# Kernel tuning notes

Measured on AMD Instinct MI355X. Metric: run time of the kernel, lower is better.

## Reference

```python
import jax, jax.numpy as jnp
import numpy as np

EMBED_DIM = 1024
NUM_HEADS = 16
HEAD_DIM = EMBED_DIM // NUM_HEADS
ROPE_BASE = 10000.0


def setup_inputs() -> dict:
    key = jax.random.key(0)
    ks = jax.random.split(key, 5)
    B, S, D = 2, 2048, EMBED_DIM
    # kaiming_uniform_(a=sqrt(5)) on [out, in] -> bound = 1/sqrt(in)
    bound = 1.0 / np.sqrt(D)
    x = jax.random.normal(ks[0], (B, S, D), dtype=jnp.float32)
    Wq = jax.random.uniform(ks[1], (D, D), dtype=jnp.float32, minval=-bound, maxval=bound)
    Wk = jax.random.uniform(ks[2], (D, D), dtype=jnp.float32, minval=-bound, maxval=bound)
    Wv = jax.random.uniform(ks[3], (D, D), dtype=jnp.float32, minval=-bound, maxval=bound)
    Wo = jax.random.uniform(ks[4], (D, D), dtype=jnp.float32, minval=-bound, maxval=bound)
    return {"x": x, "Wq": Wq, "Wk": Wk, "Wv": Wv, "Wo": Wo}


def _rope(t):
    # t: [B, H, S, hd]; standard half-split RoPE, base 10000
    hd = t.shape[-1]
    half = hd // 2
    S = t.shape[2]
    inv_freq = 1.0 / (ROPE_BASE ** (jnp.arange(half, dtype=jnp.float32) / half))
    ang = jnp.arange(S, dtype=jnp.float32)[:, None] * inv_freq[None, :]  # [S, half]
    cos, sin = jnp.cos(ang), jnp.sin(ang)
    t1, t2 = t[..., :half], t[..., half:]
    return jnp.concatenate([t1 * cos - t2 * sin, t1 * sin + t2 * cos], axis=-1)


def _attention_mc(x, Wq, Wk, Wv, Wo):
    B, S, D = x.shape
    H, hd = NUM_HEADS, HEAD_DIM
    # Linear layers: y = x @ W.T (no bias)
    q = (x @ Wq.T).reshape(B, S, H, hd).transpose(0, 2, 1, 3)  # [B,H,S,hd]
    k = (x @ Wk.T).reshape(B, S, H, hd).transpose(0, 2, 1, 3)
    v = (x @ Wv.T).reshape(B, S, H, hd).transpose(0, 2, 1, 3)
    q = _rope(q)
    k = _rope(k)
    scale = 1.0 / jnp.sqrt(jnp.float32(hd))
    scores = jnp.einsum("bhqd,bhkd->bhqk", q, k) * scale  # [B,H,S,S]
    causal = jnp.tril(jnp.ones((S, S), dtype=bool))
    scores = jnp.where(causal, scores, jnp.finfo(scores.dtype).min)
    attn = jax.nn.softmax(scores, axis=-1)
    out = jnp.einsum("bhqk,bhkd->bhqd", attn, v)  # [B,H,S,hd]
    out = out.transpose(0, 2, 1, 3).reshape(B, S, D)
    return out @ Wo.T


def reference(x, Wq, Wk, Wv, Wo):
    return _attention_mc(x, Wq, Wk, Wv, Wo)
```

## Files before the change

kernel.cpp:

```cpp
#include <hip/hip_runtime.h>
#include <math.h>
#include <stdint.h>


#define S_LEN 2048
#define NHEAD 16
#define HDIM  64
#define NBH   32

typedef __attribute__((ext_vector_type(8))) short  bf16x8;
typedef __attribute__((ext_vector_type(4))) float  f32x4;
typedef unsigned short u16;
typedef unsigned int   u32;

__device__ __forceinline__ u16 f2bf(float f) {
    u32 u = __float_as_uint(f);
    return (u16)((u + 0x7FFFu + ((u >> 16) & 1u)) >> 16);
}
__device__ __forceinline__ float bf2f(u16 s) {
    return __uint_as_float(((u32)s) << 16);
}
__device__ __forceinline__ f32x4 mfma16(bf16x8 a, bf16x8 b, f32x4 c) {
    return __builtin_amdgcn_mfma_f32_16x16x32_bf16(a, b, c, 0, 0, 0);
}
__device__ __forceinline__ void gll16(const void* g, void* l) {
    __builtin_amdgcn_global_load_lds((const __attribute__((address_space(1))) u32*)g,
                                     (__attribute__((address_space(3))) u32*)l, 16, 0, 0);
}

__global__ __launch_bounds__(256)
void split_convert(const float* __restrict__ x,
                   const float* __restrict__ Wq, const float* __restrict__ Wk,
                   const float* __restrict__ Wv, const float* __restrict__ Wo,
                   u16* __restrict__ xhi, u16* __restrict__ xlo,
                   u16* __restrict__ whi, u16* __restrict__ wlo)
{
    const int g = blockIdx.x * 256 + threadIdx.x;
    const float* src; u16 *dhi, *dlo; int loc;
    if (g < 1048576) { src = x; dhi = xhi; dlo = xlo; loc = g; }
    else {
        const int r = g - 1048576;
        const int wsel = r >> 18;
        loc = r & 262143;
        src = (wsel == 0) ? Wq : (wsel == 1) ? Wk : (wsel == 2) ? Wv : Wo;
        dhi = whi + ((size_t)wsel << 20);
        dlo = wlo + ((size_t)wsel << 20);
    }
    const float4 v = reinterpret_cast<const float4*>(src)[loc];
    ushort4 hv, lv;
    hv.x = f2bf(v.x); lv.x = f2bf(v.x - bf2f(hv.x));
    hv.y = f2bf(v.y); lv.y = f2bf(v.y - bf2f(hv.y));
    hv.z = f2bf(v.z); lv.z = f2bf(v.z - bf2f(hv.z));
    hv.w = f2bf(v.w); lv.w = f2bf(v.w - bf2f(hv.w));
    reinterpret_cast<ushort4*>(dhi)[loc] = hv;
    reinterpret_cast<ushort4*>(dlo)[loc] = lv;
}

__global__ __launch_bounds__(256)
void qkv_mfma(const u16* __restrict__ xhi, const u16* __restrict__ xlo,
              const u16* __restrict__ whi, const u16* __restrict__ wlo,
              u16* __restrict__ qhi, u16* __restrict__ qlo,
              u16* __restrict__ khi, u16* __restrict__ klo,
              u16* __restrict__ vhi, u16* __restrict__ vlo)
{
    __shared__ __align__(16) u16 Ah[4096], Al[4096], Bh[4096], Bl[4096];
    const int tid = threadIdx.x, lane = tid & 63, w = tid >> 6;
    const int l15 = lane & 15, l16 = lane >> 4;
    const int m0 = blockIdx.x * 128;
    const int ng = blockIdx.y * 128;
    const int tsel = ng >> 10;
    const int nloc0 = ng & 1023;
    const u16* __restrict__ Wh = whi + ((size_t)tsel << 20);
    const u16* __restrict__ Wl = wlo + ((size_t)tsel << 20);

    f32x4 acc[4][4];
    #pragma unroll
    for (int i = 0; i < 4; ++i)
        #pragma unroll
        for (int j = 0; j < 4; ++j) acc[i][j] = (f32x4){0.f, 0.f, 0.f, 0.f};

    for (int k0 = 0; k0 < 1024; k0 += 32) {
        __syncthreads();
        #pragma unroll
        for (int c = 0; c < 2; ++c) {
            const int idx  = w * 2 + c;
            const int trow = idx * 16 + (lane >> 2);
            const int tcol = (lane & 3) * 8;
            const size_t ga = (size_t)(m0 + trow) * 1024 + k0 + tcol;
            const size_t gb = (size_t)(nloc0 + trow) * 1024 + k0 + tcol;
            gll16(xhi + ga, (char*)Ah + idx * 1024);
            gll16(xlo + ga, (char*)Al + idx * 1024);
            gll16(Wh + gb,  (char*)Bh + idx * 1024);
            gll16(Wl + gb,  (char*)Bl + idx * 1024);
        }
        __syncthreads();
        const int mo = (w >> 1) * 64, no = (w & 1) * 64;
        bf16x8 a_h[4], a_l[4], b_h[4], b_l[4];
        #pragma unroll
        for (int f = 0; f < 4; ++f) {
            const int ao = (mo + f * 16 + l15) * 32 + l16 * 8;
            a_h[f] = *(const bf16x8*)&Ah[ao];
            a_l[f] = *(const bf16x8*)&Al[ao];
            const int bo = (no + f * 16 + l15) * 32 + l16 * 8;
            b_h[f] = *(const bf16x8*)&Bh[bo];
            b_l[f] = *(const bf16x8*)&Bl[bo];
        }
        #pragma unroll
        for (int i = 0; i < 4; ++i)
            #pragma unroll
            for (int j = 0; j < 4; ++j) {
                acc[i][j] = mfma16(a_h[i], b_h[j], acc[i][j]);
                acc[i][j] = mfma16(a_h[i], b_l[j], acc[i][j]);
                acc[i][j] = mfma16(a_l[i], b_h[j], acc[i][j]);
            }
    }

    const int mo = (w >> 1) * 64, no = (w & 1) * 64;
    const int hh = (nloc0 + no) >> 6;
    if (tsel < 2) {
        u16* __restrict__ dh = tsel ? khi : qhi;
        u16* __restrict__ dl = tsel ? klo : qlo;
        const float scl = tsel ? 1.0f : 0.125f;
        #pragma unroll
        for (int i = 0; i < 4; ++i)
            #pragma unroll
            for (int e = 0; e < 4; ++e) {
                const int row = m0 + mo + i * 16 + l16 * 4 + e;
                const int s = row & 2047, b = row >> 11;
                const size_t base = ((size_t)(b * NHEAD + hh) * S_LEN + s) * HDIM;
                #pragma unroll
                for (int j = 0; j < 2; ++j) {
                    const int d = j * 16 + l15;
                    const float inv = (float)exp((double)d * -0.28782313662425574);
                    const float ang = (float)s * inv;
                    const float sn = sinf(ang), cs = cosf(ang);
                    const float x1 = acc[i][j][e], x2 = acc[i][j + 2][e];
                    const float o1 = (x1 * cs - x2 * sn) * scl;
                    const float o2 = (x1 * sn + x2 * cs) * scl;
                    const u16 h1 = f2bf(o1), h2 = f2bf(o2);
                    dh[base + d]      = h1;
                    dl[base + d]      = f2bf(o1 - bf2f(h1));
                    dh[base + d + 32] = h2;
                    dl[base + d + 32] = f2bf(o2 - bf2f(h2));
                }
            }
    } else {
        #pragma unroll
        for (int i = 0; i < 4; ++i)
            #pragma unroll
            for (int e = 0; e < 4; ++e) {
                const int row = m0 + mo + i * 16 + l16 * 4 + e;
                const int s = row & 2047, b = row >> 11;
                const size_t base = ((size_t)(b * NHEAD + hh) * S_LEN + s) * HDIM;
                #pragma unroll
                for (int j = 0; j < 4; ++j) {
                    const float o = acc[i][j][e];
                    const u16 h1 = f2bf(o);
                    vhi[base + j * 16 + l15] = h1;
                    vlo[base + j * 16 + l15] = f2bf(o - bf2f(h1));
                }
            }
    }
}

__global__ __launch_bounds__(256)
void vtrans(const u16* __restrict__ vhi, const u16* __restrict__ vlo,
            u16* __restrict__ vthi, u16* __restrict__ vtlo)
{
    __shared__ __align__(16) u16 T[64][72];
    const u16* __restrict__ src = blockIdx.z ? vlo : vhi;
    u16* __restrict__ dst = blockIdx.z ? vtlo : vthi;
    const int bh = blockIdx.y;
    const int s0 = blockIdx.x * 64;
    const int tid = threadIdx.x;
    #pragma unroll
    for (int p = 0; p < 2; ++p) {
        const int c = tid + p * 256;
        const int r = c >> 3, dc = (c & 7) * 8;
        *(uint4*)&T[r][dc] = *(const uint4*)&src[((size_t)bh * S_LEN + s0 + r) * HDIM + dc];
    }
    __syncthreads();
    #pragma unroll
    for (int p = 0; p < 2; ++p) {
        const int c = tid + p * 256;
        const int d = c >> 3, sc8 = (c & 7) * 8;
        __align__(16) u16 tmp[8];
        #pragma unroll
        for (int u = 0; u < 8; ++u) tmp[u] = T[sc8 + u][d];
        *(uint4*)&dst[((size_t)bh * HDIM + d) * S_LEN + s0 + sc8] = *(uint4*)tmp;
    }
}

__global__ __launch_bounds__(256)
void attn_mfma(const u16* __restrict__ qhi, const u16* __restrict__ qlo,
               const u16* __restrict__ khi, const u16* __restrict__ klo,
               const u16* __restrict__ vthi, const u16* __restrict__ vtlo,
               u16* __restrict__ ohi, u16* __restrict__ olo)
{
    __shared__ __align__(16) u16 Kh[64][72], Kl[64][72], Vh[64][72], Vl[64][72];
    __shared__ __align__(16) float Pw[4][16][68];
    const int tid = threadIdx.x, lane = tid & 63, w = tid >> 6;
    const int l15 = lane & 15, l16 = lane >> 4;
    const int qt = blockIdx.x, bh = blockIdx.y;
    const size_t sbase = (size_t)bh * S_LEN * HDIM;
    const size_t dbase = (size_t)bh * HDIM * S_LEN;

    bf16x8 q_h[2], q_l[2];
    {
        const int s = qt * 64 + w * 16 + l15;
        #pragma unroll
        for (int ks = 0; ks < 2; ++ks) {
            const size_t ga = sbase + (size_t)s * HDIM + ks * 32 + l16 * 8;
            q_h[ks] = *(const bf16x8*)&qhi[ga];
            q_l[ks] = *(const bf16x8*)&qlo[ga];
        }
    }

    f32x4 oacc[4];
    #pragma unroll
    for (int t = 0; t < 4; ++t) oacc[t] = (f32x4){0.f, 0.f, 0.f, 0.f};
    float m_i[4], l_i[4];
    #pragma unroll
    for (int e = 0; e < 4; ++e) { m_i[e] = -INFINITY; l_i[e] = 0.f; }

    for (int kt = 0; kt <= qt; ++kt) {
        __syncthreads();
        #pragma unroll
        for (int p = 0; p < 2; ++p) {
            const int c = tid + p * 256;
            const int r = c >> 3, dc = (c & 7) * 8;
            const size_t gk = sbase + (size_t)(kt * 64 + r) * HDIM + dc;
            *(uint4*)&Kh[r][dc] = *(const uint4*)&khi[gk];
            *(uint4*)&Kl[r][dc] = *(const uint4*)&klo[gk];
            const size_t gv = dbase + (size_t)r * S_LEN + kt * 64 + dc;
            *(uint4*)&Vh[r][dc] = *(const uint4*)&vthi[gv];
            *(uint4*)&Vl[r][dc] = *(const uint4*)&vtlo[gv];
        }
        __syncthreads();

        f32x4 st[4];
        #pragma unroll
        for (int t = 0; t < 4; ++t) st[t] = (f32x4){0.f, 0.f, 0.f, 0.f};
        #pragma unroll
        for (int t = 0; t < 4; ++t)
            #pragma unroll
            for (int ks = 0; ks < 2; ++ks) {
                const bf16x8 kf_h = *(const bf16x8*)&Kh[t * 16 + l15][ks * 32 + l16 * 8];
                const bf16x8 kf_l = *(const bf16x8*)&Kl[t * 16 + l15][ks * 32 + l16 * 8];
                st[t] = mfma16(q_h[ks], kf_h, st[t]);
                st[t] = mfma16(q_h[ks], kf_l, st[t]);
                st[t] = mfma16(q_l[ks], kf_h, st[t]);
            }
        if (kt == qt) {
            #pragma unroll
            for (int t = 0; t < 4; ++t)
                #pragma unroll
                for (int e = 0; e < 4; ++e)
                    if (t * 16 + l15 > w * 16 + l16 * 4 + e) st[t][e] = -1e30f;
        }
        #pragma unroll
        for (int e = 0; e < 4; ++e) {
            float mx = fmaxf(fmaxf(st[0][e], st[1][e]), fmaxf(st[2][e], st[3][e]));
            #pragma unroll
            for (int msk = 8; msk >= 1; msk >>= 1) mx = fmaxf(mx, __shfl_xor(mx, msk));
            const float mn = fmaxf(m_i[e], mx);
            const float scl = __expf(m_i[e] - mn);
            float rs = 0.f;
            #pragma unroll
            for (int t = 0; t < 4; ++t) {
                const float p = __expf(st[t][e] - mn);
                st[t][e] = p; rs += p;
            }
            #pragma unroll
            for (int msk = 8; msk >= 1; msk >>= 1) rs += __shfl_xor(rs, msk);
            l_i[e] = l_i[e] * scl + rs;
            m_i[e] = mn;
            #pragma unroll
            for (int t = 0; t < 4; ++t) oacc[t][e] *= scl;
        }
        #pragma unroll
        for (int t = 0; t < 4; ++t)
            #pragma unroll
            for (int e = 0; e < 4; ++e)
                Pw[w][l16 * 4 + e][t * 16 + l15] = st[t][e];
        bf16x8 p_h[2], p_l[2];
        #pragma unroll
        for (int ks = 0; ks < 2; ++ks) {
            float pf[8];
            *(f32x4*)&pf[0] = *(const f32x4*)&Pw[w][l15][ks * 32 + l16 * 8];
            *(f32x4*)&pf[4] = *(const f32x4*)&Pw[w][l15][ks * 32 + l16 * 8 + 4];
            #pragma unroll
            for (int u = 0; u < 8; ++u) {
                const u16 hb = f2bf(pf[u]);
                p_h[ks][u] = (short)hb;
                p_l[ks][u] = (short)f2bf(pf[u] - bf2f(hb));
            }
        }
        #pragma unroll
        for (int t = 0; t < 4; ++t)
            #pragma unroll
            for (int ks = 0; ks < 2; ++ks) {
                const bf16x8 vf_h = *(const bf16x8*)&Vh[t * 16 + l15][ks * 32 + l16 * 8];
                const bf16x8 vf_l = *(const bf16x8*)&Vl[t * 16 + l15][ks * 32 + l16 * 8];
                oacc[t] = mfma16(p_h[ks], vf_h, oacc[t]);
                oacc[t] = mfma16(p_h[ks], vf_l, oacc[t]);
                oacc[t] = mfma16(p_l[ks], vf_h, oacc[t]);
            }
    }
    #pragma unroll
    for (int e = 0; e < 4; ++e) {
        const float inv = 1.f / l_i[e];
        const int s = qt * 64 + w * 16 + l16 * 4 + e;
        #pragma unroll
        for (int t = 0; t < 4; ++t) {
            const float o = oacc[t][e] * inv;
            const size_t ga = sbase + (size_t)s * HDIM + t * 16 + l15;
            const u16 hb = f2bf(o);
            ohi[ga] = hb;
            olo[ga] = f2bf(o - bf2f(hb));
        }
    }
}

__global__ __launch_bounds__(256)
void proj_mfma(const u16* __restrict__ ahi, const u16* __restrict__ alo,
               const u16* __restrict__ wohi, const u16* __restrict__ wolo,
               float* __restrict__ out)
{
    __shared__ __align__(16) u16 Ah[4096], Al[4096], Bh[4096], Bl[4096];
    const int tid = threadIdx.x, lane = tid & 63, w = tid >> 6;
    const int l15 = lane & 15, l16 = lane >> 4;
    const int m0 = blockIdx.x * 128, n0 = blockIdx.y * 128;

    f32x4 acc[4][4];
    #pragma unroll
    for (int i = 0; i < 4; ++i)
        #pragma unroll
        for (int j = 0; j < 4; ++j) acc[i][j] = (f32x4){0.f, 0.f, 0.f, 0.f};

    for (int k0 = 0; k0 < 1024; k0 += 32) {
        __syncthreads();
        #pragma unroll
        for (int c = 0; c < 2; ++c) {
            const int idx  = w * 2 + c;
            const int trow = idx * 16 + (lane >> 2);
            const int tcol = (lane & 3) * 8;
            const int ri = m0 + trow;
            const int b = ri >> 11, s = ri & 2047;
            const int kc = k0 + tcol;
            const int hh = kc >> 6, dd = kc & 63;
            const size_t ga = ((size_t)(b * NHEAD + hh) * S_LEN + s) * HDIM + dd;
            const size_t gb = (size_t)(n0 + trow) * 1024 + k0 + tcol;
            gll16(ahi + ga,  (char*)Ah + idx * 1024);
            gll16(alo + ga,  (char*)Al + idx * 1024);
            gll16(wohi + gb, (char*)Bh + idx * 1024);
            gll16(wolo + gb, (char*)Bl + idx * 1024);
        }
        __syncthreads();
        const int mo = (w >> 1) * 64, no = (w & 1) * 64;
        bf16x8 a_h[4], a_l[4], b_h[4], b_l[4];
        #pragma unroll
        for (int f = 0; f < 4; ++f) {
            const int ao = (mo + f * 16 + l15) * 32 + l16 * 8;
            a_h[f] = *(const bf16x8*)&Ah[ao];
            a_l[f] = *(const bf16x8*)&Al[ao];
            const int bo = (no + f * 16 + l15) * 32 + l16 * 8;
            b_h[f] = *(const bf16x8*)&Bh[bo];
            b_l[f] = *(const bf16x8*)&Bl[bo];
        }
        #pragma unroll
        for (int i = 0; i < 4; ++i)
            #pragma unroll
            for (int j = 0; j < 4; ++j) {
                acc[i][j] = mfma16(a_h[i], b_h[j], acc[i][j]);
                acc[i][j] = mfma16(a_h[i], b_l[j], acc[i][j]);
                acc[i][j] = mfma16(a_l[i], b_h[j], acc[i][j]);
            }
    }
    const int mo = (w >> 1) * 64, no = (w & 1) * 64;
    #pragma unroll
    for (int i = 0; i < 4; ++i)
        #pragma unroll
        for (int e = 0; e < 4; ++e) {
            const int row = m0 + mo + i * 16 + l16 * 4 + e;
            #pragma unroll
            for (int j = 0; j < 4; ++j)
                out[(size_t)row * 1024 + n0 + no + j * 16 + l15] = acc[i][j][e];
        }
}

extern "C" void kernel_launch(void* const* d_in, const int* in_sizes, int n_in,
                              void* d_out, int out_size, void* d_ws, size_t ws_size,
                              hipStream_t stream)
{
    const float* x  = (const float*)d_in[0];
    const float* Wq = (const float*)d_in[1];
    const float* Wk = (const float*)d_in[2];
    const float* Wv = (const float*)d_in[3];
    const float* Wo = (const float*)d_in[4];
    float* out = (float*)d_out;

    char* ws = (char*)d_ws;
    const size_t MB = (size_t)1 << 20;
    u16* xhi  = (u16*)(ws +  0 * MB);
    u16* xlo  = (u16*)(ws +  8 * MB);
    u16* whi  = (u16*)(ws + 16 * MB);
    u16* wlo  = (u16*)(ws + 24 * MB);
    u16* qhi  = (u16*)(ws + 32 * MB);
    u16* qlo  = (u16*)(ws + 40 * MB);
    u16* khi  = (u16*)(ws + 48 * MB);
    u16* klo  = (u16*)(ws + 56 * MB);
    u16* vhi  = (u16*)(ws + 64 * MB);
    u16* vlo  = (u16*)(ws + 72 * MB);
    u16* vthi = (u16*)(ws + 80 * MB);
    u16* vtlo = (u16*)(ws + 88 * MB);

    split_convert<<<8192, 256, 0, stream>>>(x, Wq, Wk, Wv, Wo, xhi, xlo, whi, wlo);
    qkv_mfma<<<dim3(32, 24), 256, 0, stream>>>(xhi, xlo, whi, wlo,
                                               qhi, qlo, khi, klo, vhi, vlo);
    vtrans<<<dim3(32, NBH, 2), 256, 0, stream>>>(vhi, vlo, vthi, vtlo);
    attn_mfma<<<dim3(32, NBH), 256, 0, stream>>>(qhi, qlo, khi, klo, vthi, vtlo,
                                                 xhi, xlo);
    proj_mfma<<<dim3(32, 8), 256, 0, stream>>>(xhi, xlo,
                                               whi + ((size_t)3 << 20), wlo + ((size_t)3 << 20),
                                               out);
}
```

Before: 600.0 us.

## Fuse V transpose into QKV epilogue and stage stores through LDS

The QKV GEMM epilogue now writes through shared memory so global stores of Q/K and of attention output become 16-byte coalesced rows. V is written directly in transposed layout, which removes the separate vtrans kernel and its round trip through global memory. The attention grid is also reversed so the heaviest causal query tiles launch first, for better load balance. In exchange it adds an extra barrier and an LDS staging pass in each epilogue, and the shared-memory buffers are aliased.

```diff
diff --git a/kernel.cpp b/kernel.cpp
--- a/kernel.cpp
+++ b/kernel.cpp
@@ -61,9 +61,9 @@
               const u16* __restrict__ whi, const u16* __restrict__ wlo,
               u16* __restrict__ qhi, u16* __restrict__ qlo,
               u16* __restrict__ khi, u16* __restrict__ klo,
-              u16* __restrict__ vhi, u16* __restrict__ vlo)
+              u16* __restrict__ vthi, u16* __restrict__ vtlo)
 {
-    __shared__ __align__(16) u16 Ah[4096], Al[4096], Bh[4096], Bl[4096];
+    __shared__ __align__(16) u16 SMEM[20480];
     const int tid = threadIdx.x, lane = tid & 63, w = tid >> 6;
     const int l15 = lane & 15, l16 = lane >> 4;
     const int m0 = blockIdx.x * 128;
@@ -88,10 +88,10 @@
             const int tcol = (lane & 3) * 8;
             const size_t ga = (size_t)(m0 + trow) * 1024 + k0 + tcol;
             const size_t gb = (size_t)(nloc0 + trow) * 1024 + k0 + tcol;
-            gll16(xhi + ga, (char*)Ah + idx * 1024);
-            gll16(xlo + ga, (char*)Al + idx * 1024);
-            gll16(Wh + gb,  (char*)Bh + idx * 1024);
-            gll16(Wl + gb,  (char*)Bl + idx * 1024);
+            gll16(xhi + ga, (char*)SMEM + idx * 1024);
+            gll16(xlo + ga, (char*)SMEM +  8192 + idx * 1024);
+            gll16(Wh + gb,  (char*)SMEM + 16384 + idx * 1024);
+            gll16(Wl + gb,  (char*)SMEM + 24576 + idx * 1024);
         }
         __syncthreads();
         const int mo = (w >> 1) * 64, no = (w & 1) * 64;
@@ -99,11 +99,11 @@
         #pragma unroll
         for (int f = 0; f < 4; ++f) {
             const int ao = (mo + f * 16 + l15) * 32 + l16 * 8;
-            a_h[f] = *(const bf16x8*)&Ah[ao];
-            a_l[f] = *(const bf16x8*)&Al[ao];
+            a_h[f] = *(const bf16x8*)&SMEM[ao];
+            a_l[f] = *(const bf16x8*)&SMEM[4096 + ao];
             const int bo = (no + f * 16 + l15) * 32 + l16 * 8;
-            b_h[f] = *(const bf16x8*)&Bh[bo];
-            b_l[f] = *(const bf16x8*)&Bl[bo];
+            b_h[f] = *(const bf16x8*)&SMEM[8192 + bo];
+            b_l[f] = *(const bf16x8*)&SMEM[12288 + bo];
         }
         #pragma unroll
         for (int i = 0; i < 4; ++i)
@@ -115,79 +115,84 @@
             }
     }
 
+    __syncthreads();
     const int mo = (w >> 1) * 64, no = (w & 1) * 64;
     const int hh = (nloc0 + no) >> 6;
+    const int mrow = m0 + mo;
+    const int b = mrow >> 11, sb0 = mrow & 2047;
+    u16* const chunk = SMEM + w * 5120;
+
     if (tsel < 2) {
         u16* __restrict__ dh = tsel ? khi : qhi;
         u16* __restrict__ dl = tsel ? klo : qlo;
         const float scl = tsel ? 1.0f : 0.125f;
-        #pragma unroll
-        for (int i = 0; i < 4; ++i)
-            #pragma unroll
-            for (int e = 0; e < 4; ++e) {
-                const int row = m0 + mo + i * 16 + l16 * 4 + e;
-                const int s = row & 2047, b = row >> 11;
-                const size_t base = ((size_t)(b * NHEAD + hh) * S_LEN + s) * HDIM;
+        const float inv0 = (float)exp((double)l15        * -0.28782313662425574);
+        const float inv1 = (float)exp((double)(l15 + 16) * -0.28782313662425574);
+        u16* const Thi = chunk;
+        u16* const Tlo = chunk + 2304;
+        #pragma unroll
+        for (int half = 0; half < 2; ++half) {
+            #pragma unroll
+            for (int i2 = 0; i2 < 2; ++i2) {
+                const int i = half * 2 + i2;
                 #pragma unroll
-                for (int j = 0; j < 2; ++j) {
-                    const int d = j * 16 + l15;
-                    const float inv = (float)exp((double)d * -0.28782313662425574);
-                    const float ang = (float)s * inv;
-                    const float sn = sinf(ang), cs = cosf(ang);
-                    const float x1 = acc[i][j][e], x2 = acc[i][j + 2][e];
-                    const float o1 = (x1 * cs - x2 * sn) * scl;
-                    const float o2 = (x1 * sn + x2 * cs) * scl;
-                    const u16 h1 = f2bf(o1), h2 = f2bf(o2);
-                    dh[base + d]      = h1;
-                    dl[base + d]      = f2bf(o1 - bf2f(h1));
-                    dh[base + d + 32] = h2;
-                    dl[base + d + 32] = f2bf(o2 - bf2f(h2));
+                for (int e = 0; e < 4; ++e) {
+                    const int rl = i2 * 16 + l16 * 4 + e;
+                    const int s = sb0 + half * 32 + rl;
+                    #pragma unroll
+                    for (int j = 0; j < 2; ++j) {
+                        const float inv = j ? inv1 : inv0;
+                        const float ang = (float)s * inv;
+                        const float sn = sinf(ang), cs = cosf(ang);
+                        const float x1 = acc[i][j][e], x2 = acc[i][j + 2][e];
+                        const float o1 = (x1 * cs - x2 * sn) * scl;
+                        const float o2 = (x1 * sn + x2 * cs) * scl;
+                        const u16 h1 = f2bf(o1), h2 = f2bf(o2);
+                        Thi[rl * 72 + j * 16 + l15]       = h1;
+                        Tlo[rl * 72 + j * 16 + l15]       = f2bf(o1 - bf2f(h1));
+                        Thi[rl * 72 + (j + 2) * 16 + l15] = h2;
+                        Tlo[rl * 72 + (j + 2) * 16 + l15] = f2bf(o2 - bf2f(h2));
+                    }
                 }
             }
+            #pragma unroll
+            for (int p = 0; p < 4; ++p) {
+                const int slot = p * 64 + lane;
+                const int rr = slot >> 3, c8 = (slot & 7) * 8;
+                const size_t ga = (((size_t)(b * NHEAD + hh) * S_LEN) + sb0 + half * 32 + rr) * HDIM + c8;
+                *(uint4*)&dh[ga] = *(const uint4*)&Thi[rr * 72 + c8];
+                *(uint4*)&dl[ga] = *(const uint4*)&Tlo[rr * 72 + c8];
+            }
+        }
     } else {
-        #pragma unroll
-        for (int i = 0; i < 4; ++i)
-            #pragma unroll
-            for (int e = 0; e < 4; ++e) {
-                const int row = m0 + mo + i * 16 + l16 * 4 + e;
-                const int s = row & 2047, b = row >> 11;
-                const size_t base = ((size_t)(b * NHEAD + hh) * S_LEN + s) * HDIM;
+        u16* const Thi = chunk;
+        u16* const Tlo = chunk + 2560;
+        #pragma unroll
+        for (int half = 0; half < 2; ++half) {
+            #pragma unroll
+            for (int i2 = 0; i2 < 2; ++i2) {
+                const int i = half * 2 + i2;
                 #pragma unroll
-                for (int j = 0; j < 4; ++j) {
-                    const float o = acc[i][j][e];
-                    const u16 h1 = f2bf(o);
-                    vhi[base + j * 16 + l15] = h1;
-                    vlo[base + j * 16 + l15] = f2bf(o - bf2f(h1));
+                for (int e = 0; e < 4; ++e) {
+                    const int rl = i2 * 16 + l16 * 4 + e;
+                    #pragma unroll
+                    for (int j = 0; j < 4; ++j) {
+                        const float o = acc[i][j][e];
+                        const u16 hb = f2bf(o);
+                        Thi[(j * 16 + l15) * 40 + rl] = hb;
+                        Tlo[(j * 16 + l15) * 40 + rl] = f2bf(o - bf2f(hb));
+                    }
                 }
             }
-    }
-}
-
-__global__ __launch_bounds__(256)
-void vtrans(const u16* __restrict__ vhi, const u16* __restrict__ vlo,
-            u16* __restrict__ vthi, u16* __restrict__ vtlo)
-{
-    __shared__ __align__(16) u16 T[64][72];
-    const u16* __restrict__ src = blockIdx.z ? vlo : vhi;
-    u16* __restrict__ dst = blockIdx.z ? vtlo : vthi;
-    const int bh = blockIdx.y;
-    const int s0 = blockIdx.x * 64;
-    const int tid = threadIdx.x;
-    #pragma unroll
-    for (int p = 0; p < 2; ++p) {
-        const int c = tid + p * 256;
-        const int r = c >> 3, dc = (c & 7) * 8;
-        *(uint4*)&T[r][dc] = *(const uint4*)&src[((size_t)bh * S_LEN + s0 + r) * HDIM + dc];
-    }
-    __syncthreads();
-    #pragma unroll
-    for (int p = 0; p < 2; ++p) {
-        const int c = tid + p * 256;
-        const int d = c >> 3, sc8 = (c & 7) * 8;
-        __align__(16) u16 tmp[8];
-        #pragma unroll
-        for (int u = 0; u < 8; ++u) tmp[u] = T[sc8 + u][d];
-        *(uint4*)&dst[((size_t)bh * HDIM + d) * S_LEN + s0 + sc8] = *(uint4*)tmp;
+            #pragma unroll
+            for (int p = 0; p < 4; ++p) {
+                const int slot = p * 64 + lane;
+                const int dd = slot >> 2, s8 = (slot & 3) * 8;
+                const size_t ga = (((size_t)(b * NHEAD + hh) * HDIM) + dd) * S_LEN + sb0 + half * 32 + s8;
+                *(uint4*)&vthi[ga] = *(const uint4*)&Thi[dd * 40 + s8];
+                *(uint4*)&vtlo[ga] = *(const uint4*)&Tlo[dd * 40 + s8];
+            }
+        }
     }
 }
 
@@ -197,13 +202,19 @@
                const u16* __restrict__ vthi, const u16* __restrict__ vtlo,
                u16* __restrict__ ohi, u16* __restrict__ olo)
 {
-    __shared__ __align__(16) u16 Kh[64][72], Kl[64][72], Vh[64][72], Vl[64][72];
-    __shared__ __align__(16) float Pw[4][16][68];
+    __shared__ __align__(16) u16 AS[27136];
+    u16* const KH = AS;
+    u16* const KL = AS + 4608;
+    u16* const VH = AS + 9216;
+    u16* const VL = AS + 13824;
+    float* const PW = (float*)(AS + 18432);
     const int tid = threadIdx.x, lane = tid & 63, w = tid >> 6;
     const int l15 = lane & 15, l16 = lane >> 4;
-    const int qt = blockIdx.x, bh = blockIdx.y;
+    const int qt = 31 - blockIdx.x;
+    const int bh = blockIdx.y;
     const size_t sbase = (size_t)bh * S_LEN * HDIM;
     const size_t dbase = (size_t)bh * HDIM * S_LEN;
+    float* const pw = PW + w * 1088;
 
     bf16x8 q_h[2], q_l[2];
     {
@@ -230,11 +241,11 @@
             const int c = tid + p * 256;
             const int r = c >> 3, dc = (c & 7) * 8;
             const size_t gk = sbase + (size_t)(kt * 64 + r) * HDIM + dc;
-            *(uint4*)&Kh[r][dc] = *(const uint4*)&khi[gk];
-            *(uint4*)&Kl[r][dc] = *(const uint4*)&klo[gk];
+            *(uint4*)&KH[r * 72 + dc] = *(const uint4*)&khi[gk];
+            *(uint4*)&KL[r * 72 + dc] = *(const uint4*)&klo[gk];
             const size_t gv = dbase + (size_t)r * S_LEN + kt * 64 + dc;
-            *(uint4*)&Vh[r][dc] = *(const uint4*)&vthi[gv];
-            *(uint4*)&Vl[r][dc] = *(const uint4*)&vtlo[gv];
+            *(uint4*)&VH[r * 72 + dc] = *(const uint4*)&vthi[gv];
+            *(uint4*)&VL[r * 72 + dc] = *(const uint4*)&vtlo[gv];
         }
         __syncthreads();
 
@@ -245,8 +256,8 @@
         for (int t = 0; t < 4; ++t)
             #pragma unroll
             for (int ks = 0; ks < 2; ++ks) {
-                const bf16x8 kf_h = *(const bf16x8*)&Kh[t * 16 + l15][ks * 32 + l16 * 8];
-                const bf16x8 kf_l = *(const bf16x8*)&Kl[t * 16 + l15][ks * 32 + l16 * 8];
+                const bf16x8 kf_h = *(const bf16x8*)&KH[(t * 16 + l15) * 72 + ks * 32 + l16 * 8];
+                const bf16x8 kf_l = *(const bf16x8*)&KL[(t * 16 + l15) * 72 + ks * 32 + l16 * 8];
                 st[t] = mfma16(q_h[ks], kf_h, st[t]);
                 st[t] = mfma16(q_h[ks], kf_l, st[t]);
                 st[t] = mfma16(q_l[ks], kf_h, st[t]);
@@ -282,13 +293,13 @@
         for (int t = 0; t < 4; ++t)
             #pragma unroll
             for (int e = 0; e < 4; ++e)
-                Pw[w][l16 * 4 + e][t * 16 + l15] = st[t][e];
+                pw[(l16 * 4 + e) * 68 + t * 16 + l15] = st[t][e];
         bf16x8 p_h[2], p_l[2];
         #pragma unroll
         for (int ks = 0; ks < 2; ++ks) {
             float pf[8];
-            *(f32x4*)&pf[0] = *(const f32x4*)&Pw[w][l15][ks * 32 + l16 * 8];
-            *(f32x4*)&pf[4] = *(const f32x4*)&Pw[w][l15][ks * 32 + l16 * 8 + 4];
+            *(f32x4*)&pf[0] = *(const f32x4*)&pw[l15 * 68 + ks * 32 + l16 * 8];
+            *(f32x4*)&pf[4] = *(const f32x4*)&pw[l15 * 68 + ks * 32 + l16 * 8 + 4];
             #pragma unroll
             for (int u = 0; u < 8; ++u) {
                 const u16 hb = f2bf(pf[u]);
@@ -300,25 +311,35 @@
         for (int t = 0; t < 4; ++t)
             #pragma unroll
             for (int ks = 0; ks < 2; ++ks) {
-                const bf16x8 vf_h = *(const bf16x8*)&Vh[t * 16 + l15][ks * 32 + l16 * 8];
-                const bf16x8 vf_l = *(const bf16x8*)&Vl[t * 16 + l15][ks * 32 + l16 * 8];
+                const bf16x8 vf_h = *(const bf16x8*)&VH[(t * 16 + l15) * 72 + ks * 32 + l16 * 8];
+                const bf16x8 vf_l = *(const bf16x8*)&VL[(t * 16 + l15) * 72 + ks * 32 + l16 * 8];
                 oacc[t] = mfma16(p_h[ks], vf_h, oacc[t]);
                 oacc[t] = mfma16(p_h[ks], vf_l, oacc[t]);
                 oacc[t] = mfma16(p_l[ks], vf_h, oacc[t]);
             }
     }
+    __syncthreads();
+    u16* const Ohi = AS + w * 2304;
+    u16* const Olo = Ohi + 1152;
     #pragma unroll
     for (int e = 0; e < 4; ++e) {
-        const float inv = 1.f / l_i[e];
-        const int s = qt * 64 + w * 16 + l16 * 4 + e;
+        const float invl = 1.f / l_i[e];
+        const int rl = l16 * 4 + e;
         #pragma unroll
         for (int t = 0; t < 4; ++t) {
-            const float o = oacc[t][e] * inv;
-            const size_t ga = sbase + (size_t)s * HDIM + t * 16 + l15;
+            const float o = oacc[t][e] * invl;
             const u16 hb = f2bf(o);
-            ohi[ga] = hb;
-            olo[ga] = f2bf(o - bf2f(hb));
-        }
+            Ohi[rl * 72 + t * 16 + l15] = hb;
+            Olo[rl * 72 + t * 16 + l15] = f2bf(o - bf2f(hb));
+        }
+    }
+    #pragma unroll
+    for (int p = 0; p < 2; ++p) {
+        const int slot = p * 64 + lane;
+        const int rr = slot >> 3, c8 = (slot & 7) * 8;
+        const size_t ga = sbase + (size_t)(qt * 64 + w * 16 + rr) * HDIM + c8;
+        *(uint4*)&ohi[ga] = *(const uint4*)&Ohi[rr * 72 + c8];
+        *(uint4*)&olo[ga] = *(const uint4*)&Olo[rr * 72 + c8];
     }
 }
 
@@ -410,15 +431,12 @@
     u16* qlo  = (u16*)(ws + 40 * MB);
     u16* khi  = (u16*)(ws + 48 * MB);
     u16* klo  = (u16*)(ws + 56 * MB);
-    u16* vhi  = (u16*)(ws + 64 * MB);
-    u16* vlo  = (u16*)(ws + 72 * MB);
-    u16* vthi = (u16*)(ws + 80 * MB);
-    u16* vtlo = (u16*)(ws + 88 * MB);
+    u16* vthi = (u16*)(ws + 64 * MB);
+    u16* vtlo = (u16*)(ws + 72 * MB);
 
     split_convert<<<8192, 256, 0, stream>>>(x, Wq, Wk, Wv, Wo, xhi, xlo, whi, wlo);
     qkv_mfma<<<dim3(32, 24), 256, 0, stream>>>(xhi, xlo, whi, wlo,
-                                               qhi, qlo, khi, klo, vhi, vlo);
-    vtrans<<<dim3(32, NBH, 2), 256, 0, stream>>>(vhi, vlo, vthi, vtlo);
+                                               qhi, qlo, khi, klo, vthi, vtlo);
     attn_mfma<<<dim3(32, NBH), 256, 0, stream>>>(qhi, qlo, khi, klo, vthi, vtlo,
                                                  xhi, xlo);
     proj_mfma<<<dim3(32, 8), 256, 0, stream>>>(xhi, xlo,
```

New measurement: 599.9 us. Within noise of the previous version (-0.0%).
